# Kernel optimization log

Measured on AMD Instinct MI355X. Metric: run time of the kernel, lower is better.

The kernel has to match this reference:

```python
import jax, jax.numpy as jnp
import numpy as np

H = 8
D_MODEL = 512
D_K = D_MODEL // H
B = 8
S = 1024


def _linear(x, W, b):
    # torch nn.Linear: y = x @ W.T + b, W: [out, in]
    return jnp.einsum('bsd,ed->bse', x, W) + b


def _to_heads(x):
    # [B,S,D] -> [B,H,S,d_k]
    return x.reshape(B, S, H, D_K).transpose(0, 2, 1, 3)


def setup_inputs() -> dict:
    key = jax.random.key(0)
    ks = jax.random.split(key, 20)
    inp = {
        'input_rgb': jax.random.normal(ks[0], (B, S, D_MODEL), jnp.float32),
        'input_flow': jax.random.normal(ks[1], (B, S, D_MODEL), jnp.float32),
    }
    names = ['Wq1', 'Wk1', 'Wv1', 'Wq2', 'Wk2', 'Wv2', 'Wo1', 'Wo2']
    for i, n in enumerate(names):
        inp[n] = jax.random.normal(ks[2 + i], (D_MODEL, D_MODEL), jnp.float32) * 0.02
        inp['b' + n[1:]] = jax.random.normal(ks[10 + i], (D_MODEL,), jnp.float32) * 0.02
    return inp


def reference(input_rgb, input_flow, Wq1, bq1, Wk1, bk1, Wv1, bv1,
              Wq2, bq2, Wk2, bk2, Wv2, bv2, Wo1, bo1, Wo2, bo2):
    scale = 1.0 / jnp.sqrt(jnp.asarray(D_K, input_rgb.dtype))

    q_r = _to_heads(_linear(input_rgb, Wq1, bq1))
    k_r = _to_heads(_linear(input_rgb, Wk1, bk1))
    v_r = _to_heads(_linear(input_rgb, Wv1, bv1))
    q_f = _to_heads(_linear(input_flow, Wq2, bq2))
    k_f = _to_heads(_linear(input_flow, Wk2, bk2))
    v_f = _to_heads(_linear(input_flow, Wv2, bv2))

    # two full [B,H,S,S] softmax attention maps
    attn_rgb = jax.nn.softmax(jnp.einsum('bhqd,bhkd->bhqk', q_r, k_r) * scale, axis=-1)
    attn_flow = jax.nn.softmax(jnp.einsum('bhqd,bhkd->bhqk', q_f, k_f) * scale, axis=-1)
    # elementwise max merge (breaks flash-attention fusion)
    attn = jnp.maximum(attn_rgb, attn_flow)

    # Attention2: out = attn @ value (dropout is identity in eval mode)
    out_rgb = jnp.einsum('bhqk,bhkd->bhqd', attn, v_r)
    out_flow = jnp.einsum('bhqk,bhkd->bhqd', attn, v_f)

    out_rgb = out_rgb.transpose(0, 2, 1, 3).reshape(B, S, D_MODEL)
    out_flow = out_flow.transpose(0, 2, 1, 3).reshape(B, S, D_MODEL)
    return (_linear(out_rgb, Wo1, bo1), _linear(out_flow, Wo2, bo2))
```

## Files before the change

### kernel.cpp

```cpp
#include <hip/hip_runtime.h>
#include <hip/hip_bf16.h>


typedef unsigned short u16;
typedef __attribute__((ext_vector_type(8))) short short8;
typedef __attribute__((ext_vector_type(4))) short s4pack;
typedef __attribute__((ext_vector_type(4))) float floatx4;

#define B_DIM 8
#define S_DIM 1024
#define H_DIM 8
#define DK 64
#define DMODEL 512
#define NTOK (B_DIM * S_DIM)
#define SEG ((size_t)NTOK * DMODEL)
#define WSEG ((size_t)DMODEL * DMODEL)

#define SCHED_FENCE() __builtin_amdgcn_sched_barrier(0)
#define LGKM0() asm volatile("s_waitcnt lgkmcnt(0)" ::: "memory")
#define VMCNT0() asm volatile("s_waitcnt vmcnt(0)" ::: "memory")
#define BARRIER() __builtin_amdgcn_s_barrier()

__device__ __forceinline__ floatx4 mfma_bf16(short8 a, short8 b, floatx4 c) {
  return __builtin_amdgcn_mfma_f32_16x16x32_bf16(a, b, c, 0, 0, 0);
}

__device__ __forceinline__ u16 f32_to_bf16_rne(float f) {
  unsigned u = __float_as_uint(f);
  unsigned r = u + 0x7FFFu + ((u >> 16) & 1u);
  return (u16)(r >> 16);
}

__device__ __forceinline__ float bf16_bits_to_f32(u16 u) {
  return __uint_as_float(((unsigned)u) << 16);
}

__device__ __forceinline__ void async_cp16(const u16* g, u16* lds) {
  __builtin_amdgcn_global_load_lds(
      (__attribute__((address_space(1))) void*)(const_cast<u16*>(g)),
      (__attribute__((address_space(3))) void*)(lds), 16, 0, 0);
}

#define NT_CONV 18
struct ConvParams {
  const void* src[NT_CONV];
  u16* dst[NT_CONV];
  int n[NT_CONV];
  int coff[NT_CONV + 1];
};

__global__ __launch_bounds__(256) void convert_inputs(ConvParams p) {
  __shared__ int flag_f32;
  const int blk = blockIdx.x;
  int t = 0;
  while (t + 1 < NT_CONV && blk >= p.coff[t + 1]) ++t;
  const int lc = blk - p.coff[t];
  const int n = p.n[t];
  const int tid = threadIdx.x;

  if (tid < 64) {
    const u16* s = (const u16*)p.src[t];
    int bad = 0;
#pragma unroll
    for (int j = 0; j < 8; ++j) {
      float f = bf16_bits_to_f32(s[tid * 8 + j]);
      bad |= !(fabsf(f) < 1e4f);
    }
    bad |= __shfl_xor(bad, 1);
    bad |= __shfl_xor(bad, 2);
    bad |= __shfl_xor(bad, 4);
    bad |= __shfl_xor(bad, 8);
    bad |= __shfl_xor(bad, 16);
    bad |= __shfl_xor(bad, 32);
    if (tid == 0) flag_f32 = bad;
  }
  __syncthreads();
  const int is_f32 = flag_f32;
  const int base = lc * 65536;

  for (int it = 0; it < 32; ++it) {
    const int idx = base + (it * 256 + tid) * 8;
    if (idx + 8 > n) break;
    if (!is_f32) {
      *(short8*)&p.dst[t][idx] = *(const short8*)&((const u16*)p.src[t])[idx];
    } else {
      const float* s = (const float*)p.src[t] + idx;
      short8 o;
#pragma unroll
      for (int j = 0; j < 8; ++j) o[j] = (short)f32_to_bf16_rne(s[j]);
      *(short8*)&p.dst[t][idx] = o;
    }
  }
}

__device__ __forceinline__ void gemm128_mainloop(
    const u16* __restrict__ A, const u16* __restrict__ W,
    int m0, int n0, int K, u16* ldsA, u16* ldsB, floatx4 acc[4][4]) {
  const int tid = threadIdx.x;
  const int lane = tid & 63;
  const int wid = tid >> 6;
  const int wm = wid >> 1, wn = wid & 1;
  const int r = lane & 15, g = lane >> 4;

  const int stg_row = wid * 32 + (lane >> 2);
  const int stg_col = (lane & 3) * 8;

  const u16* ga0 = A + (size_t)(m0 + stg_row) * K + stg_col;
  const u16* ga1 = A + (size_t)(m0 + stg_row + 16) * K + stg_col;
  const u16* gb0 = W + (size_t)(n0 + stg_row) * K + stg_col;
  const u16* gb1 = W + (size_t)(n0 + stg_row + 16) * K + stg_col;
  const int lo0 = (wid * 32) * 32;
  const int lo1 = (wid * 32 + 16) * 32;

  async_cp16(ga0, ldsA + lo0);
  async_cp16(ga1, ldsA + lo1);
  async_cp16(gb0, ldsB + lo0);
  async_cp16(gb1, ldsB + lo1);
  VMCNT0();
  BARRIER();

  int cur = 0;
  for (int k0 = 0; k0 < K; k0 += 32) {
    const int nxt = cur ^ 1;
    const bool more = (k0 + 32 < K);
    if (more) {
      const int nb = nxt * 4096;
      async_cp16(ga0 + k0 + 32, ldsA + nb + lo0);
      async_cp16(ga1 + k0 + 32, ldsA + nb + lo1);
      async_cp16(gb0 + k0 + 32, ldsB + nb + lo0);
      async_cp16(gb1 + k0 + 32, ldsB + nb + lo1);
    }
    const int cb = cur * 4096;
    short8 a[4], b[4];
#pragma unroll
    for (int i = 0; i < 4; ++i)
      a[i] = *(const short8*)&ldsA[cb + (wm * 64 + i * 16 + r) * 32 + g * 8];
#pragma unroll
    for (int j = 0; j < 4; ++j)
      b[j] = *(const short8*)&ldsB[cb + (wn * 64 + j * 16 + r) * 32 + g * 8];
#pragma unroll
    for (int i = 0; i < 4; ++i)
#pragma unroll
      for (int j = 0; j < 4; ++j)
        acc[i][j] = mfma_bf16(a[i], b[j], acc[i][j]);
    if (more) {
      SCHED_FENCE(); VMCNT0(); BARRIER(); SCHED_FENCE();
      cur = nxt;
    }
  }
}

struct QkvParams {
  const u16* X[2];
  const u16* W[2][3];
  const u16* Bias[2][3];
  u16* Out[2][3];
};

__global__ __launch_bounds__(256) void qkv_gemm(QkvParams p) {
  __shared__ u16 ldsA[2 * 128 * 32];
  __shared__ u16 ldsB[2 * 128 * 32];
  const int z = blockIdx.z;
  const int wi = blockIdx.y >> 2;
  const int n0 = (blockIdx.y & 3) * 128;
  const int m0 = blockIdx.x * 128;

  floatx4 acc[4][4];
  const floatx4 z4 = {0.f, 0.f, 0.f, 0.f};
#pragma unroll
  for (int i = 0; i < 4; ++i)
#pragma unroll
    for (int j = 0; j < 4; ++j) acc[i][j] = z4;

  gemm128_mainloop(p.X[z], p.W[z][wi], m0, n0, DMODEL, ldsA, ldsB, acc);

  const int tid = threadIdx.x, lane = tid & 63, wid = tid >> 6;
  const int wm = wid >> 1, wn = wid & 1, r = lane & 15, g = lane >> 4;
  const u16* bias = p.Bias[z][wi];
  u16* out = p.Out[z][wi];
  const float qscale = 0.125f * 1.4426950408889634f;

#pragma unroll
  for (int j = 0; j < 4; ++j) {
    const int c = n0 + wn * 64 + j * 16 + r;
    const float bv = bf16_bits_to_f32(bias[c]);
    const int h = c >> 6, d = c & 63;
#pragma unroll
    for (int i = 0; i < 4; ++i) {
      const int row0 = m0 + wm * 64 + i * 16 + g * 4;
      const int bb = row0 >> 10, ss0 = row0 & 1023;
      if (wi == 2) {
        s4pack pk;
#pragma unroll
        for (int ii = 0; ii < 4; ++ii)
          pk[ii] = (short)f32_to_bf16_rne(acc[i][j][ii] + bv);
        *(s4pack*)&out[(((size_t)(bb * H_DIM + h)) * DK + d) * S_DIM + ss0] = pk;
      } else {
#pragma unroll
        for (int ii = 0; ii < 4; ++ii) {
          float v = acc[i][j][ii] + bv;
          if (wi == 0) v *= qscale;
          out[(((size_t)(bb * H_DIM + h)) * S_DIM + (ss0 + ii)) * DK + d] =
              f32_to_bf16_rne(v);
        }
      }
    }
  }
}

#define KVB 32
#define QB 64

struct AttnParams {
  const u16* Q[2];
  const u16* K[2];
  const u16* Vt[2];
  u16* O[2];
};

__global__ __launch_bounds__(256, 4) void attn_merged(AttnParams p) {
  __shared__ u16 Ks[2][KVB * 64];
  __shared__ u16 Vs[2][64 * KVB];
  __shared__ u16 Ps[QB * 40];

  const int tid = threadIdx.x;
  const int lane = tid & 63;
  const int wid = tid >> 6;
  const int r = lane & 15, g = lane >> 4;

  const int lin = blockIdx.x;
  const int w = (lin & 7) * 128 + (lin >> 3);
  const int bh = w >> 4;
  const int q0 = (w & 15) * QB;
  const size_t hbase = (size_t)bh * S_DIM * DK;

  const int krow = tid >> 3, kch = tid & 7;
  const int kdst = krow * 64 + ((kch ^ (krow & 7)) * 8);
  const size_t kgsrc = (size_t)krow * DK + kch * 8;
  const int vrow = tid >> 2, vch = tid & 3;
  const int vdst = vrow * KVB + ((vch ^ ((vrow >> 2) & 3)) * 8);
  const size_t vgsrc = (size_t)vrow * S_DIM + vch * 8;

  short8 qf[2][2];
#pragma unroll
  for (int s = 0; s < 2; ++s)
#pragma unroll
    for (int kc = 0; kc < 2; ++kc)
      qf[s][kc] = *(const short8*)
          &p.Q[s][hbase + (size_t)(q0 + wid * 16 + r) * DK + kc * 32 + g * 8];

  short8 kst[2], vst[2];
#pragma unroll
  for (int s = 0; s < 2; ++s)
    kst[s] = *(const short8*)&p.K[s][hbase + kgsrc];

  float sums[2][4];
#pragma unroll
  for (int s = 0; s < 2; ++s)
#pragma unroll
    for (int i = 0; i < 4; ++i) sums[s][i] = 0.f;

  for (int kt = 0; kt < 32; ++kt) {
    if (kt) { SCHED_FENCE(); BARRIER(); SCHED_FENCE(); }
#pragma unroll
    for (int s = 0; s < 2; ++s)
      *(short8*)&Ks[s][kdst] = kst[s];
    if (kt < 31) {
      const size_t k0n = (size_t)(kt + 1) * KVB * DK;
#pragma unroll
      for (int s = 0; s < 2; ++s)
        kst[s] = *(const short8*)&p.K[s][hbase + k0n + kgsrc];
    }
    SCHED_FENCE(); LGKM0(); BARRIER(); SCHED_FENCE();

#pragma unroll
    for (int s = 0; s < 2; ++s)
#pragma unroll
      for (int nt = 0; nt < 2; ++nt) {
        const int row = nt * 16 + r;
        const short8 b0 = *(const short8*)&Ks[s][row * 64 + ((g ^ (r & 7)) * 8)];
        const short8 b1 =
            *(const short8*)&Ks[s][row * 64 + (((4 + g) ^ (r & 7)) * 8)];
        floatx4 acc = {0.f, 0.f, 0.f, 0.f};
        acc = mfma_bf16(qf[s][0], b0, acc);
        acc = mfma_bf16(qf[s][1], b1, acc);
#pragma unroll
        for (int i = 0; i < 4; ++i)
          sums[s][i] += __builtin_amdgcn_exp2f(acc[i]);
      }
  }

#pragma unroll
  for (int s = 0; s < 2; ++s) {
    kst[s] = *(const short8*)&p.K[s][hbase + kgsrc];
    vst[s] = *(const short8*)&p.Vt[s][hbase + vgsrc];
  }

  float inv_[2][4];
#pragma unroll
  for (int s = 0; s < 2; ++s)
#pragma unroll
    for (int i = 0; i < 4; ++i) {
      float v = sums[s][i];
      v += __shfl_xor(v, 1);
      v += __shfl_xor(v, 2);
      v += __shfl_xor(v, 4);
      v += __shfl_xor(v, 8);
      inv_[s][i] = 1.0f / v;
    }

  floatx4 o_[2][4];
  const floatx4 z4 = {0.f, 0.f, 0.f, 0.f};
#pragma unroll
  for (int s = 0; s < 2; ++s)
#pragma unroll
    for (int nt = 0; nt < 4; ++nt) o_[s][nt] = z4;

  for (int kt = 0; kt < 32; ++kt) {
    SCHED_FENCE(); BARRIER(); SCHED_FENCE();
#pragma unroll
    for (int s = 0; s < 2; ++s) {
      *(short8*)&Ks[s][kdst] = kst[s];
      *(short8*)&Vs[s][vdst] = vst[s];
    }
    if (kt < 31) {
      const size_t kn = (size_t)(kt + 1) * KVB;
#pragma unroll
      for (int s = 0; s < 2; ++s) {
        kst[s] = *(const short8*)&p.K[s][hbase + kn * DK + kgsrc];
        vst[s] = *(const short8*)&p.Vt[s][hbase + vgsrc + kn];
      }
    }
    SCHED_FENCE(); LGKM0(); BARRIER(); SCHED_FENCE();

#pragma unroll
    for (int nt = 0; nt < 2; ++nt) {
      const int row = nt * 16 + r;
      const short8 br0 = *(const short8*)&Ks[0][row * 64 + ((g ^ (r & 7)) * 8)];
      const short8 br1 =
          *(const short8*)&Ks[0][row * 64 + (((4 + g) ^ (r & 7)) * 8)];
      const short8 bf0 = *(const short8*)&Ks[1][row * 64 + ((g ^ (r & 7)) * 8)];
      const short8 bf1 =
          *(const short8*)&Ks[1][row * 64 + (((4 + g) ^ (r & 7)) * 8)];
      floatx4 ar = {0.f, 0.f, 0.f, 0.f};
      floatx4 af = {0.f, 0.f, 0.f, 0.f};
      ar = mfma_bf16(qf[0][0], br0, ar);
      ar = mfma_bf16(qf[0][1], br1, ar);
      af = mfma_bf16(qf[1][0], bf0, af);
      af = mfma_bf16(qf[1][1], bf1, af);
      const int prow = wid * 16 + g * 4;
#pragma unroll
      for (int i = 0; i < 4; ++i) {
        const float pr = __builtin_amdgcn_exp2f(ar[i]) * inv_[0][i];
        const float pf = __builtin_amdgcn_exp2f(af[i]) * inv_[1][i];
        Ps[(prow + i) * 40 + nt * 16 + r] = f32_to_bf16_rne(fmaxf(pr, pf));
      }
    }

    LGKM0();
    SCHED_FENCE();

    const short8 pa = *(const short8*)&Ps[(wid * 16 + r) * 40 + g * 8];
#pragma unroll
    for (int s = 0; s < 2; ++s)
#pragma unroll
      for (int nt = 0; nt < 4; ++nt) {
        const int vr = nt * 16 + r;
        const short8 v = *(const short8*)
            &Vs[s][vr * KVB + ((g ^ ((r >> 2) & 3)) * 8)];
        o_[s][nt] = mfma_bf16(pa, v, o_[s][nt]);
      }
  }

  const int bb = bh >> 3, h = bh & 7;
#pragma unroll
  for (int s = 0; s < 2; ++s) {
    u16* out = p.O[s];
#pragma unroll
    for (int nt = 0; nt < 4; ++nt) {
      const int col = h * 64 + nt * 16 + r;
#pragma unroll
      for (int i = 0; i < 4; ++i) {
        const int row = q0 + wid * 16 + g * 4 + i;
        out[((size_t)bb * S_DIM + row) * DMODEL + col] =
            f32_to_bf16_rne(o_[s][nt][i]);
      }
    }
  }
}

struct OutParams {
  const u16* A[2];
  const u16* W[2];
  const u16* Bias[2];
  float* Out[2];
};

__global__ __launch_bounds__(256) void out_gemm(OutParams p) {
  __shared__ u16 ldsA[2 * 128 * 32];
  __shared__ u16 ldsB[2 * 128 * 32];
  const int z = blockIdx.z;
  const int m0 = blockIdx.x * 128;
  const int n0 = blockIdx.y * 128;

  floatx4 acc[4][4];
  const floatx4 z4 = {0.f, 0.f, 0.f, 0.f};
#pragma unroll
  for (int i = 0; i < 4; ++i)
#pragma unroll
    for (int j = 0; j < 4; ++j) acc[i][j] = z4;

  gemm128_mainloop(p.A[z], p.W[z], m0, n0, DMODEL, ldsA, ldsB, acc);

  const int tid = threadIdx.x, lane = tid & 63, wid = tid >> 6;
  const int wm = wid >> 1, wn = wid & 1, r = lane & 15, g = lane >> 4;
  const u16* bias = p.Bias[z];
  float* out = p.Out[z];

#pragma unroll
  for (int j = 0; j < 4; ++j) {
    const int c = n0 + wn * 64 + j * 16 + r;
    const float bv = bf16_bits_to_f32(bias[c]);
#pragma unroll
    for (int i = 0; i < 4; ++i) {
      const int row0 = m0 + wm * 64 + i * 16 + g * 4;
#pragma unroll
      for (int ii = 0; ii < 4; ++ii)
        out[(size_t)(row0 + ii) * DMODEL + c] = acc[i][j][ii] + bv;
    }
  }
}

extern "C" void kernel_launch(void* const* d_in, const int* in_sizes, int n_in,
                              void* d_out, int out_size, void* d_ws, size_t ws_size,
                              hipStream_t stream) {
  (void)in_sizes; (void)n_in; (void)out_size; (void)ws_size;
  u16* ws = (u16*)d_ws;
  u16* Qr = ws + 0 * SEG;
  u16* Kr = ws + 1 * SEG;
  u16* Vr = ws + 2 * SEG;
  u16* Qf = ws + 3 * SEG;
  u16* Kf = ws + 4 * SEG;
  u16* Vf = ws + 5 * SEG;
  u16* Or = ws + 6 * SEG;
  u16* Of = ws + 7 * SEG;
  u16* cW = ws + 8 * SEG;
  u16* cB = cW + 8 * WSEG;

  ConvParams cp;
  int coff = 0;
  for (int i = 0; i < NT_CONV; ++i) {
    cp.src[i] = d_in[i];
    int n;
    if (i < 2) {
      n = (int)SEG;
      cp.dst[i] = (i == 0) ? Or : Of;
    } else {
      const int k = (i - 2) >> 1;
      const int isb = (i - 2) & 1;
      n = isb ? DMODEL : (int)WSEG;
      cp.dst[i] = isb ? (cB + k * DMODEL) : (cW + k * WSEG);
    }
    cp.n[i] = n;
    cp.coff[i] = coff;
    coff += (n + 65535) / 65536;
  }
  cp.coff[NT_CONV] = coff;
  convert_inputs<<<dim3(coff), dim3(256), 0, stream>>>(cp);

  QkvParams qp;
  qp.X[0] = Or;
  qp.X[1] = Of;
  for (int s = 0; s < 2; ++s)
    for (int wi = 0; wi < 3; ++wi) {
      const int k = s * 3 + wi;
      qp.W[s][wi] = cW + k * WSEG;
      qp.Bias[s][wi] = cB + k * DMODEL;
    }
  qp.Out[0][0] = Qr; qp.Out[0][1] = Kr; qp.Out[0][2] = Vr;
  qp.Out[1][0] = Qf; qp.Out[1][1] = Kf; qp.Out[1][2] = Vf;
  qkv_gemm<<<dim3(64, 12, 2), dim3(256), 0, stream>>>(qp);

  AttnParams ap;
  ap.Q[0] = Qr; ap.Q[1] = Qf;
  ap.K[0] = Kr; ap.K[1] = Kf;
  ap.Vt[0] = Vr; ap.Vt[1] = Vf;
  ap.O[0] = Or; ap.O[1] = Of;
  attn_merged<<<dim3(1024), dim3(256), 0, stream>>>(ap);

  OutParams op;
  op.A[0] = Or; op.A[1] = Of;
  op.W[0] = cW + 6 * WSEG; op.Bias[0] = cB + 6 * DMODEL;
  op.W[1] = cW + 7 * WSEG; op.Bias[1] = cB + 7 * DMODEL;
  op.Out[0] = (float*)d_out;
  op.Out[1] = (float*)d_out + SEG;
  out_gemm<<<dim3(64, 4, 2), dim3(256), 0, stream>>>(op);
}
```

Before: 280.7 us.

## Rewrite merged attention to split KV across waves with register-direct K/V loads

The attention kernel now assigns each wave a slice of the key sequence instead of a slice of queries. Each wave loads K and transposed V fragments straight from global memory into registers, so the LDS staging, per-tile barriers and the P round-trip through shared memory are gone. P is fed to 16x16x16 MFMAs directly from the accumulator layout. Partial outputs and row sums are reduced across waves through LDS at the end. The GEMM kernels also get a flattened grid with an XCD-aware block remap. In exchange the kernel uses far more registers (occupancy hint drops to 2), needs a cross-wave reduction epilogue, and relies on uncoalesced narrow global V loads.

```diff
diff --git a/kernel.cpp b/kernel.cpp
--- a/kernel.cpp
+++ b/kernel.cpp
@@ -17,12 +17,16 @@
 #define WSEG ((size_t)DMODEL * DMODEL)
 
 #define SCHED_FENCE() __builtin_amdgcn_sched_barrier(0)
-#define LGKM0() asm volatile("s_waitcnt lgkmcnt(0)" ::: "memory")
 #define VMCNT0() asm volatile("s_waitcnt vmcnt(0)" ::: "memory")
 #define BARRIER() __builtin_amdgcn_s_barrier()
 
 __device__ __forceinline__ floatx4 mfma_bf16(short8 a, short8 b, floatx4 c) {
   return __builtin_amdgcn_mfma_f32_16x16x32_bf16(a, b, c, 0, 0, 0);
+}
+
+__device__ __forceinline__ void mfma16(floatx4& c, s4pack a, s4pack b) {
+  asm volatile("v_mfma_f32_16x16x16_bf16 %0, %1, %2, %0"
+               : "+v"(c) : "v"(a), "v"(b));
 }
 
 __device__ __forceinline__ u16 f32_to_bf16_rne(float f) {
@@ -160,10 +164,14 @@
 __global__ __launch_bounds__(256) void qkv_gemm(QkvParams p) {
   __shared__ u16 ldsA[2 * 128 * 32];
   __shared__ u16 ldsB[2 * 128 * 32];
-  const int z = blockIdx.z;
-  const int wi = blockIdx.y >> 2;
-  const int n0 = (blockIdx.y & 3) * 128;
-  const int m0 = blockIdx.x * 128;
+  const int lin = blockIdx.x;
+  const int wg = (lin & 7) * 192 + (lin >> 3);
+  const int m0 = (wg / 24) * 128;
+  const int c = wg % 24;
+  const int z = c / 12;
+  const int yc = c % 12;
+  const int wi = yc >> 2;
+  const int n0 = (yc & 3) * 128;
 
   floatx4 acc[4][4];
   const floatx4 z4 = {0.f, 0.f, 0.f, 0.f};
@@ -182,9 +190,9 @@
 
 #pragma unroll
   for (int j = 0; j < 4; ++j) {
-    const int c = n0 + wn * 64 + j * 16 + r;
-    const float bv = bf16_bits_to_f32(bias[c]);
-    const int h = c >> 6, d = c & 63;
+    const int cc = n0 + wn * 64 + j * 16 + r;
+    const float bv = bf16_bits_to_f32(bias[cc]);
+    const int h = cc >> 6, d = cc & 63;
 #pragma unroll
     for (int i = 0; i < 4; ++i) {
       const int row0 = m0 + wm * 64 + i * 16 + g * 4;
@@ -208,7 +216,6 @@
   }
 }
 
-#define KVB 32
 #define QB 64
 
 struct AttnParams {
@@ -218,10 +225,9 @@
   u16* O[2];
 };
 
-__global__ __launch_bounds__(256, 4) void attn_merged(AttnParams p) {
-  __shared__ u16 Ks[2][KVB * 64];
-  __shared__ u16 Vs[2][64 * KVB];
-  __shared__ u16 Ps[QB * 40];
+__global__ __launch_bounds__(256, 2) void attn_merged(AttnParams p) {
+  __shared__ float ored[2][2][QB][DK];
+  __shared__ float sred[2][4][16][4];
 
   const int tid = threadIdx.x;
   const int lane = tid & 63;
@@ -234,158 +240,182 @@
   const int q0 = (w & 15) * QB;
   const size_t hbase = (size_t)bh * S_DIM * DK;
 
-  const int krow = tid >> 3, kch = tid & 7;
-  const int kdst = krow * 64 + ((kch ^ (krow & 7)) * 8);
-  const size_t kgsrc = (size_t)krow * DK + kch * 8;
-  const int vrow = tid >> 2, vch = tid & 3;
-  const int vdst = vrow * KVB + ((vch ^ ((vrow >> 2) & 3)) * 8);
-  const size_t vgsrc = (size_t)vrow * S_DIM + vch * 8;
-
-  short8 qf[2][2];
+  const u16* __restrict__ Kp0 = p.K[0] + hbase;
+  const u16* __restrict__ Kp1 = p.K[1] + hbase;
+  const u16* __restrict__ Vp0 = p.Vt[0] + hbase;
+  const u16* __restrict__ Vp1 = p.Vt[1] + hbase;
+
+  short8 qf[2][4][2];
 #pragma unroll
   for (int s = 0; s < 2; ++s)
 #pragma unroll
-    for (int kc = 0; kc < 2; ++kc)
-      qf[s][kc] = *(const short8*)
-          &p.Q[s][hbase + (size_t)(q0 + wid * 16 + r) * DK + kc * 32 + g * 8];
-
-  short8 kst[2], vst[2];
+    for (int mt = 0; mt < 4; ++mt)
+#pragma unroll
+      for (int kc = 0; kc < 2; ++kc)
+        qf[s][mt][kc] = *(const short8*)
+            &p.Q[s][hbase + (size_t)(q0 + mt * 16 + r) * DK + kc * 32 + g * 8];
+
+  const int koff = (wid * 16 + r) * DK + g * 8;
+  const floatx4 z4 = {0.f, 0.f, 0.f, 0.f};
+
+  short8 kA[2][2];
+  kA[0][0] = *(const short8*)&Kp0[koff];
+  kA[0][1] = *(const short8*)&Kp0[koff + 32];
+  kA[1][0] = *(const short8*)&Kp1[koff];
+  kA[1][1] = *(const short8*)&Kp1[koff + 32];
+
+  float sl[2][4];
 #pragma unroll
   for (int s = 0; s < 2; ++s)
-    kst[s] = *(const short8*)&p.K[s][hbase + kgsrc];
-
-  float sums[2][4];
+#pragma unroll
+    for (int mt = 0; mt < 4; ++mt) sl[s][mt] = 0.f;
+
+  for (int kt = 0; kt < 16; ++kt) {
+#pragma unroll
+    for (int mt = 0; mt < 4; ++mt) {
+      floatx4 ar = mfma_bf16(kA[0][0], qf[0][mt][0], z4);
+      ar = mfma_bf16(kA[0][1], qf[0][mt][1], ar);
+      floatx4 af = mfma_bf16(kA[1][0], qf[1][mt][0], z4);
+      af = mfma_bf16(kA[1][1], qf[1][mt][1], af);
+      sl[0][mt] += __builtin_amdgcn_exp2f(ar[0]) + __builtin_amdgcn_exp2f(ar[1]) +
+                   __builtin_amdgcn_exp2f(ar[2]) + __builtin_amdgcn_exp2f(ar[3]);
+      sl[1][mt] += __builtin_amdgcn_exp2f(af[0]) + __builtin_amdgcn_exp2f(af[1]) +
+                   __builtin_amdgcn_exp2f(af[2]) + __builtin_amdgcn_exp2f(af[3]);
+    }
+    if (kt < 15) {
+      const int kn = (kt + 1) * 64 * DK + koff;
+      kA[0][0] = *(const short8*)&Kp0[kn];
+      kA[0][1] = *(const short8*)&Kp0[kn + 32];
+      kA[1][0] = *(const short8*)&Kp1[kn];
+      kA[1][1] = *(const short8*)&Kp1[kn + 32];
+    }
+  }
+
 #pragma unroll
   for (int s = 0; s < 2; ++s)
 #pragma unroll
-    for (int i = 0; i < 4; ++i) sums[s][i] = 0.f;
-
-  for (int kt = 0; kt < 32; ++kt) {
-    if (kt) { SCHED_FENCE(); BARRIER(); SCHED_FENCE(); }
+    for (int mt = 0; mt < 4; ++mt) {
+      float v = sl[s][mt];
+      v += __shfl_xor(v, 16);
+      v += __shfl_xor(v, 32);
+      if (g == 0) sred[s][mt][r][wid] = v;
+    }
+  __syncthreads();
+
+  kA[0][0] = *(const short8*)&Kp0[koff];
+  kA[0][1] = *(const short8*)&Kp0[koff + 32];
+  kA[1][0] = *(const short8*)&Kp1[koff];
+  kA[1][1] = *(const short8*)&Kp1[koff + 32];
+
+  float inv_[2][4];
+#pragma unroll
+  for (int s = 0; s < 2; ++s)
+#pragma unroll
+    for (int mt = 0; mt < 4; ++mt) {
+      const floatx4 sv = *(const floatx4*)&sred[s][mt][r][0];
+      inv_[s][mt] = 1.0f / (sv[0] + sv[1] + sv[2] + sv[3]);
+    }
+
+  floatx4 o_[2][4][4];
+#pragma unroll
+  for (int s = 0; s < 2; ++s)
+#pragma unroll
+    for (int mt = 0; mt < 4; ++mt)
+#pragma unroll
+      for (int nt = 0; nt < 4; ++nt) o_[s][mt][nt] = z4;
+
+  const int voff = r * S_DIM + wid * 16 + g * 4;
+
+  for (int kt = 0; kt < 16; ++kt) {
+    s4pack vB[2][4];
+#pragma unroll
+    for (int nt = 0; nt < 4; ++nt) {
+      const int va = voff + nt * 16 * S_DIM + kt * 64;
+      vB[0][nt] = *(const s4pack*)&Vp0[va];
+      vB[1][nt] = *(const s4pack*)&Vp1[va];
+    }
+
+    s4pack pA[4];
+#pragma unroll
+    for (int mt = 0; mt < 4; ++mt) {
+      floatx4 ar = mfma_bf16(kA[0][0], qf[0][mt][0], z4);
+      ar = mfma_bf16(kA[0][1], qf[0][mt][1], ar);
+      floatx4 af = mfma_bf16(kA[1][0], qf[1][mt][0], z4);
+      af = mfma_bf16(kA[1][1], qf[1][mt][1], af);
+#pragma unroll
+      for (int i = 0; i < 4; ++i) {
+        const float pr = __builtin_amdgcn_exp2f(ar[i]) * inv_[0][mt];
+        const float pf = __builtin_amdgcn_exp2f(af[i]) * inv_[1][mt];
+        pA[mt][i] = (short)f32_to_bf16_rne(fmaxf(pr, pf));
+      }
+    }
+
+    if (kt < 15) {
+      const int kn = (kt + 1) * 64 * DK + koff;
+      kA[0][0] = *(const short8*)&Kp0[kn];
+      kA[0][1] = *(const short8*)&Kp0[kn + 32];
+      kA[1][0] = *(const short8*)&Kp1[kn];
+      kA[1][1] = *(const short8*)&Kp1[kn + 32];
+    }
+
+    asm volatile("s_nop 7" :::);
+#pragma unroll
+    for (int mt = 0; mt < 4; ++mt)
+#pragma unroll
+      for (int nt = 0; nt < 4; ++nt) {
+        mfma16(o_[0][mt][nt], pA[mt], vB[0][nt]);
+        mfma16(o_[1][mt][nt], pA[mt], vB[1][nt]);
+      }
+  }
+
+  if (wid < 2) {
 #pragma unroll
     for (int s = 0; s < 2; ++s)
-      *(short8*)&Ks[s][kdst] = kst[s];
-    if (kt < 31) {
-      const size_t k0n = (size_t)(kt + 1) * KVB * DK;
-#pragma unroll
-      for (int s = 0; s < 2; ++s)
-        kst[s] = *(const short8*)&p.K[s][hbase + k0n + kgsrc];
-    }
-    SCHED_FENCE(); LGKM0(); BARRIER(); SCHED_FENCE();
-
+#pragma unroll
+      for (int mt = 0; mt < 4; ++mt)
+#pragma unroll
+        for (int nt = 0; nt < 4; ++nt)
+#pragma unroll
+          for (int i = 0; i < 4; ++i)
+            ored[wid][s][mt * 16 + g * 4 + i][nt * 16 + r] = o_[s][mt][nt][i];
+  }
+  __syncthreads();
+  if (wid >= 2) {
 #pragma unroll
     for (int s = 0; s < 2; ++s)
 #pragma unroll
-      for (int nt = 0; nt < 2; ++nt) {
-        const int row = nt * 16 + r;
-        const short8 b0 = *(const short8*)&Ks[s][row * 64 + ((g ^ (r & 7)) * 8)];
-        const short8 b1 =
-            *(const short8*)&Ks[s][row * 64 + (((4 + g) ^ (r & 7)) * 8)];
-        floatx4 acc = {0.f, 0.f, 0.f, 0.f};
-        acc = mfma_bf16(qf[s][0], b0, acc);
-        acc = mfma_bf16(qf[s][1], b1, acc);
-#pragma unroll
-        for (int i = 0; i < 4; ++i)
-          sums[s][i] += __builtin_amdgcn_exp2f(acc[i]);
-      }
-  }
-
+      for (int mt = 0; mt < 4; ++mt)
+#pragma unroll
+        for (int nt = 0; nt < 4; ++nt)
+#pragma unroll
+          for (int i = 0; i < 4; ++i)
+            ored[wid - 2][s][mt * 16 + g * 4 + i][nt * 16 + r] += o_[s][mt][nt][i];
+  }
+  __syncthreads();
+
+  const int q = tid >> 2, ds0 = (tid & 3) * 16;
+  const int bb = bh >> 3, h = bh & 7;
 #pragma unroll
   for (int s = 0; s < 2; ++s) {
-    kst[s] = *(const short8*)&p.K[s][hbase + kgsrc];
-    vst[s] = *(const short8*)&p.Vt[s][hbase + vgsrc];
-  }
-
-  float inv_[2][4];
-#pragma unroll
-  for (int s = 0; s < 2; ++s)
-#pragma unroll
-    for (int i = 0; i < 4; ++i) {
-      float v = sums[s][i];
-      v += __shfl_xor(v, 1);
-      v += __shfl_xor(v, 2);
-      v += __shfl_xor(v, 4);
-      v += __shfl_xor(v, 8);
-      inv_[s][i] = 1.0f / v;
-    }
-
-  floatx4 o_[2][4];
-  const floatx4 z4 = {0.f, 0.f, 0.f, 0.f};
-#pragma unroll
-  for (int s = 0; s < 2; ++s)
-#pragma unroll
-    for (int nt = 0; nt < 4; ++nt) o_[s][nt] = z4;
-
-  for (int kt = 0; kt < 32; ++kt) {
-    SCHED_FENCE(); BARRIER(); SCHED_FENCE();
-#pragma unroll
-    for (int s = 0; s < 2; ++s) {
-      *(short8*)&Ks[s][kdst] = kst[s];
-      *(short8*)&Vs[s][vdst] = vst[s];
-    }
-    if (kt < 31) {
-      const size_t kn = (size_t)(kt + 1) * KVB;
-#pragma unroll
-      for (int s = 0; s < 2; ++s) {
-        kst[s] = *(const short8*)&p.K[s][hbase + kn * DK + kgsrc];
-        vst[s] = *(const short8*)&p.Vt[s][hbase + vgsrc + kn];
-      }
-    }
-    SCHED_FENCE(); LGKM0(); BARRIER(); SCHED_FENCE();
-
-#pragma unroll
-    for (int nt = 0; nt < 2; ++nt) {
-      const int row = nt * 16 + r;
-      const short8 br0 = *(const short8*)&Ks[0][row * 64 + ((g ^ (r & 7)) * 8)];
-      const short8 br1 =
-          *(const short8*)&Ks[0][row * 64 + (((4 + g) ^ (r & 7)) * 8)];
-      const short8 bf0 = *(const short8*)&Ks[1][row * 64 + ((g ^ (r & 7)) * 8)];
-      const short8 bf1 =
-          *(const short8*)&Ks[1][row * 64 + (((4 + g) ^ (r & 7)) * 8)];
-      floatx4 ar = {0.f, 0.f, 0.f, 0.f};
-      floatx4 af = {0.f, 0.f, 0.f, 0.f};
-      ar = mfma_bf16(qf[0][0], br0, ar);
-      ar = mfma_bf16(qf[0][1], br1, ar);
-      af = mfma_bf16(qf[1][0], bf0, af);
-      af = mfma_bf16(qf[1][1], bf1, af);
-      const int prow = wid * 16 + g * 4;
-#pragma unroll
-      for (int i = 0; i < 4; ++i) {
-        const float pr = __builtin_amdgcn_exp2f(ar[i]) * inv_[0][i];
-        const float pf = __builtin_amdgcn_exp2f(af[i]) * inv_[1][i];
-        Ps[(prow + i) * 40 + nt * 16 + r] = f32_to_bf16_rne(fmaxf(pr, pf));
-      }
-    }
-
-    LGKM0();
-    SCHED_FENCE();
-
-    const short8 pa = *(const short8*)&Ps[(wid * 16 + r) * 40 + g * 8];
-#pragma unroll
-    for (int s = 0; s < 2; ++s)
-#pragma unroll
-      for (int nt = 0; nt < 4; ++nt) {
-        const int vr = nt * 16 + r;
-        const short8 v = *(const short8*)
-            &Vs[s][vr * KVB + ((g ^ ((r >> 2) & 3)) * 8)];
-        o_[s][nt] = mfma_bf16(pa, v, o_[s][nt]);
-      }
-  }
-
-  const int bb = bh >> 3, h = bh & 7;
-#pragma unroll
-  for (int s = 0; s < 2; ++s) {
-    u16* out = p.O[s];
-#pragma unroll
-    for (int nt = 0; nt < 4; ++nt) {
-      const int col = h * 64 + nt * 16 + r;
-#pragma unroll
-      for (int i = 0; i < 4; ++i) {
-        const int row = q0 + wid * 16 + g * 4 + i;
-        out[((size_t)bb * S_DIM + row) * DMODEL + col] =
-            f32_to_bf16_rne(o_[s][nt][i]);
-      }
-    }
+    floatx4 v0 = *(const floatx4*)&ored[0][s][q][ds0 + 0];
+    floatx4 v1 = *(const floatx4*)&ored[0][s][q][ds0 + 4];
+    floatx4 v2 = *(const floatx4*)&ored[0][s][q][ds0 + 8];
+    floatx4 v3 = *(const floatx4*)&ored[0][s][q][ds0 + 12];
+    v0 += *(const floatx4*)&ored[1][s][q][ds0 + 0];
+    v1 += *(const floatx4*)&ored[1][s][q][ds0 + 4];
+    v2 += *(const floatx4*)&ored[1][s][q][ds0 + 8];
+    v3 += *(const floatx4*)&ored[1][s][q][ds0 + 12];
+    short8 lo, hi;
+#pragma unroll
+    for (int k = 0; k < 4; ++k) {
+      lo[k] = (short)f32_to_bf16_rne(v0[k]);
+      lo[4 + k] = (short)f32_to_bf16_rne(v1[k]);
+      hi[k] = (short)f32_to_bf16_rne(v2[k]);
+      hi[4 + k] = (short)f32_to_bf16_rne(v3[k]);
+    }
+    u16* out = p.O[s] + ((size_t)(bb * S_DIM + q0 + q)) * DMODEL + h * 64 + ds0;
+    *(short8*)&out[0] = lo;
+    *(short8*)&out[8] = hi;
   }
 }
 
@@ -399,9 +429,12 @@
 __global__ __launch_bounds__(256) void out_gemm(OutParams p) {
   __shared__ u16 ldsA[2 * 128 * 32];
   __shared__ u16 ldsB[2 * 128 * 32];
-  const int z = blockIdx.z;
-  const int m0 = blockIdx.x * 128;
-  const int n0 = blockIdx.y * 128;
+  const int lin = blockIdx.x;
+  const int wg = (lin & 7) * 64 + (lin >> 3);
+  const int m0 = (wg >> 3) * 128;
+  const int c = wg & 7;
+  const int z = c >> 2;
+  const int n0 = (c & 3) * 128;
 
   floatx4 acc[4][4];
   const floatx4 z4 = {0.f, 0.f, 0.f, 0.f};
@@ -419,14 +452,14 @@
 
 #pragma unroll
   for (int j = 0; j < 4; ++j) {
-    const int c = n0 + wn * 64 + j * 16 + r;
-    const float bv = bf16_bits_to_f32(bias[c]);
+    const int cc = n0 + wn * 64 + j * 16 + r;
+    const float bv = bf16_bits_to_f32(bias[cc]);
 #pragma unroll
     for (int i = 0; i < 4; ++i) {
       const int row0 = m0 + wm * 64 + i * 16 + g * 4;
 #pragma unroll
       for (int ii = 0; ii < 4; ++ii)
-        out[(size_t)(row0 + ii) * DMODEL + c] = acc[i][j][ii] + bv;
+        out[(size_t)(row0 + ii) * DMODEL + cc] = acc[i][j][ii] + bv;
     }
   }
 }
@@ -479,7 +512,7 @@
     }
   qp.Out[0][0] = Qr; qp.Out[0][1] = Kr; qp.Out[0][2] = Vr;
   qp.Out[1][0] = Qf; qp.Out[1][1] = Kf; qp.Out[1][2] = Vf;
-  qkv_gemm<<<dim3(64, 12, 2), dim3(256), 0, stream>>>(qp);
+  qkv_gemm<<<dim3(1536), dim3(256), 0, stream>>>(qp);
 
   AttnParams ap;
   ap.Q[0] = Qr; ap.Q[1] = Qf;
@@ -494,5 +527,5 @@
   op.W[1] = cW + 7 * WSEG; op.Bias[1] = cB + 7 * DMODEL;
   op.Out[0] = (float*)d_out;
   op.Out[1] = (float*)d_out + SEG;
-  out_gemm<<<dim3(64, 4, 2), dim3(256), 0, stream>>>(op);
-}
+  out_gemm<<<dim3(512), dim3(256), 0, stream>>>(op);
+}
```

After: 403.1 us. 43.6% more time.
